# Optimization experiments

Hardware: AMD Instinct MI355X
Metric: run time of the kernel (lower is better)

The kernel has to match this reference:

```python
import jax, jax.numpy as jnp
import numpy as np

EPS = 1e-12
N_WAY, N_SHOT, C_IN, H_IN, W_IN = 5, 5, 640, 24, 24
TOP_LR = 0.8


def _normalize(x, axis):
    # torch F.normalize: x / max(||x||_2, eps)
    n = jnp.sqrt(jnp.sum(x * x, axis=axis, keepdims=True))
    return x / jnp.maximum(n, EPS)


def _conv1x1(x, W, b):
    # x: (B,C,H,W), W: (O,C), b: (O,)
    return jnp.einsum('bchw,oc->bohw', x, W) + b[None, :, None, None]


def _attlayer(x, Wc, bc, Wq, bq, Wk, bk):
    B, C, H, W = x.shape
    HW = H * W
    n_way, n_shot = N_WAY, N_SHOT
    scale = 1.0 / (C ** 0.5)
    x5 = _conv1x1(x, Wc, bc) + x
    x5 = _conv1x1(x5, Wq, bq)            # note: query_transform applied here
    # query_transform applied AGAIN (faithful to original)
    xq = _conv1x1(x5, Wq, bq).reshape(n_way, n_shot, C, HW)
    x_query = jnp.swapaxes(xq, 2, 3).reshape(n_way, n_shot * HW, C)
    xk = _conv1x1(x5, Wk, bk).reshape(n_way, n_shot, C, HW)
    x_key = jnp.swapaxes(xk, 1, 2).reshape(n_way, C, n_shot * HW)
    x_w1 = jnp.matmul(x_query, x_key) * scale          # (n_way, n_shot*HW, n_shot*HW)
    x_w = x_w1.reshape(n_way, n_shot * HW, n_shot, HW).max(-1).mean(-1)
    x_w = jax.nn.softmax(x_w.reshape(n_way, n_shot, HW), axis=-1)
    norm0 = _normalize(x5, 1).reshape(n_way, n_shot, C, H, W)
    # hard-max mask over spatial positions
    mask = (x_w == x_w.max(-1, keepdims=True)).astype(x.dtype)   # (n_way, n_shot, HW)
    seeds = (norm0 * mask.reshape(n_way, n_shot, 1, H, W)).sum((3, 4))  # (n_way, n_shot, C)
    # conv3d with 1x1 spatial kernel over full channel depth == einsum
    cor = jnp.einsum('nkcyx,okc->noyx', norm0, seeds).reshape(n_way, n_shot, HW)
    cmin = cor.min(-1, keepdims=True)
    cmax = cor.max(-1, keepdims=True)
    cor = (cor - cmin) / (cmax - cmin + EPS)
    cormap = cor.reshape(n_way * n_shot, 1, H, W)
    x51 = (x5 * cormap).reshape(n_way, n_shot, C, H, W)
    return x51.mean((1, 3, 4))  # (n_way, C)


def _cdsnet(lf):
    B, C, H, W = lf.shape
    HW = H * W
    n_way, n_shot = N_WAY, N_SHOT
    lfn = _normalize(lf, 1)
    X = jnp.swapaxes(lfn.reshape(B, C, HW), 1, 2)          # (B, HW, C)
    intra = X.reshape(n_way, n_shot * HW, C)
    # d_intra: masked (1-eye) gram mean == (x_i . S_way - ||x_i||^2)/(n_shot*HW)
    S_way = intra.sum(1)                                    # (n_way, C)
    d_intra = (jnp.einsum('nic,nc->ni', intra, S_way) - (intra * intra).sum(-1)) / (n_shot * HW)
    # d_inter: block-diagonal (same-image) pairs masked out
    S_tot = X.sum((0, 1))                                   # (C,)
    S_img = X.sum(1)                                        # (B, C)
    d_inter = (jnp.einsum('bic,c->bi', X, S_tot) - jnp.einsum('bic,bc->bi', X, S_img)) / (B * HW)
    cds = jax.nn.sigmoid(d_intra.reshape(n_way, -1) / d_inter.reshape(n_way, -1))  # (n_way, n_shot*HW)
    k = int(n_shot * HW * TOP_LR)
    _, sel_idx = jax.lax.top_k(cds, k)
    sel = jnp.zeros((n_way, n_shot * HW), lf.dtype)
    sel = sel.at[jnp.arange(n_way)[:, None], sel_idx].set(1.0)
    pos_small = sel.reshape(n_way * n_shot, 1, H, W)
    slf = lf * pos_small                                    # select_local_features
    slf_n = jnp.swapaxes(_normalize(slf.reshape(B, C, HW), 1), 1, 2)
    slf_n = slf_n.reshape(n_way, n_shot, HW, C)
    m1 = slf_n.reshape(n_way, n_shot * HW, C).mean(1)       # (n_way, C)
    l_intra = jnp.matmul(m1, m1.T) * (1.0 - jnp.eye(n_way, dtype=lf.dtype))
    m2 = slf_n.mean(2)                                      # (n_way, n_shot, C)
    l_inter = jnp.einsum('nsc,ntc->nst', m2, m2) * (1.0 - jnp.eye(n_shot, dtype=lf.dtype))
    loss = jnp.exp(l_inter.mean() / l_intra.mean())
    pos_index = jnp.broadcast_to(pos_small, (B, C, H, W))
    neg_index = 1.0 - pos_index
    return loss, pos_index, neg_index


def setup_inputs() -> dict:
    key = jax.random.key(0)
    ks = jax.random.split(key, 7)
    C = C_IN
    s = N_WAY * N_SHOT
    scale = 1.0 / np.sqrt(C)
    lf = jax.random.normal(ks[0], (s, C, H_IN, W_IN), jnp.float32)
    Wc = jax.random.normal(ks[1], (C, C), jnp.float32) * scale
    bc = jax.random.normal(ks[2], (C,), jnp.float32) * 0.01
    Wq = jax.random.normal(ks[3], (C, C), jnp.float32) * scale
    bq = jax.random.normal(ks[4], (C,), jnp.float32) * 0.01
    Wk = jax.random.normal(ks[5], (C, C), jnp.float32) * scale
    bk = jax.random.normal(ks[6], (C,), jnp.float32) * 0.01
    return {'local_feature': lf, 'Wc': Wc, 'bc': bc, 'Wq': Wq, 'bq': bq, 'Wk': Wk, 'bk': bk}


def reference(local_feature, Wc, bc, Wq, bq, Wk, bk):
    s, c, h, w = local_feature.shape
    hw = h * w
    proto1 = _attlayer(local_feature, Wc, bc, Wq, bq, Wk, bk)   # (n_way, C)
    global_proto = jnp.broadcast_to(proto1[:, None, :], (N_WAY, N_SHOT, c)).reshape(s, c)
    gpa = global_proto[:, None, :]                               # (s, 1, C) -> broadcasts to (s, HW, C)
    contrastive_loss, pos_index, neg_index = _cdsnet(local_feature)
    pos_x = _normalize(jnp.swapaxes((local_feature * pos_index).reshape(s, c, hw), 1, 2), -1)
    neg_x = _normalize(jnp.swapaxes((local_feature * neg_index).reshape(s, c, hw), 1, 2), -1)
    pos_value = jnp.exp(pos_x * gpa).sum(-1).mean(-1).mean(-1)
    neg_value = jnp.exp(neg_x * gpa).sum(-1).mean(-1).mean(-1)
    ctc_loss = -jnp.log(pos_value / neg_value)
    return (contrastive_loss, ctc_loss, pos_index)
```

## Files before the change

### kernel.cpp

```cpp
#include <hip/hip_runtime.h>
#include <math.h>

#define NW 5
#define NS 5
#define BB 25
#define CD 640
#define HWD 576
#define NP 2880
#define KTOP 2304
#define EPSF 1e-12f

typedef __attribute__((ext_vector_type(8))) short short8;
typedef __attribute__((ext_vector_type(4))) float f32x4;

__device__ inline unsigned short f2bf(float x) {
    unsigned u = __float_as_uint(x);
    return (unsigned short)((u + 0x7fffu + ((u >> 16) & 1u)) >> 16);
}
__device__ inline float bf2f(unsigned short h) { return __uint_as_float(((unsigned)h) << 16); }

__device__ inline void gload_lds16(const void* g, void* l) {
    __builtin_amdgcn_global_load_lds(
        (const __attribute__((address_space(1))) unsigned int*)g,
        (__attribute__((address_space(3))) unsigned int*)l, 16, 0, 0);
}

__device__ void dev_gemm640(const float* __restrict__ A, const float* __restrict__ B,
                            const float* __restrict__ add, float* __restrict__ C,
                            unsigned short* __restrict__ H, unsigned short* __restrict__ L,
                            int mode, int bx, int by, char* smem)
{
    float (*At)[68] = (float(*)[68])smem;
    float (*Bt)[64] = (float(*)[64])(smem + 8704);
    const int o0 = by * 64, j0 = bx * 64;
    const int t  = threadIdx.x;
    const int to = (t >> 4) * 4, tj = (t & 15) * 4;

    float acc[4][4];
#pragma unroll
    for (int r = 0; r < 4; ++r)
#pragma unroll
        for (int s = 0; s < 4; ++s) acc[r][s] = 0.f;

    for (int c0 = 0; c0 < CD; c0 += 32) {
        __syncthreads();
        {
            const int r = t >> 3, c8 = (t & 7) * 8;
            float4 b0 = *(const float4*)&B[(size_t)(c0+r)*CD + j0 + c8];
            float4 b1 = *(const float4*)&B[(size_t)(c0+r)*CD + j0 + c8 + 4];
            *(float4*)&Bt[r][c8]     = b0;
            *(float4*)&Bt[r][c8 + 4] = b1;
            if (mode == 0) {
                float4 a0 = *(const float4*)&A[(size_t)(c0+r)*CD + o0 + c8];
                float4 a1 = *(const float4*)&A[(size_t)(c0+r)*CD + o0 + c8 + 4];
                *(float4*)&At[r][c8]     = a0;
                *(float4*)&At[r][c8 + 4] = a1;
            } else {
                const int r2 = t >> 2, c82 = (t & 3) * 8;
                float4 a0 = *(const float4*)&A[(size_t)(o0+r2)*CD + c0 + c82];
                float4 a1 = *(const float4*)&A[(size_t)(o0+r2)*CD + c0 + c82 + 4];
                At[c82+0][r2] = a0.x; At[c82+1][r2] = a0.y;
                At[c82+2][r2] = a0.z; At[c82+3][r2] = a0.w;
                At[c82+4][r2] = a1.x; At[c82+5][r2] = a1.y;
                At[c82+6][r2] = a1.z; At[c82+7][r2] = a1.w;
            }
        }
        __syncthreads();
#pragma unroll
        for (int kk = 0; kk < 32; ++kk) {
            float4 av = *(const float4*)&At[kk][to];
            float4 bv = *(const float4*)&Bt[kk][tj];
            float aa[4] = {av.x, av.y, av.z, av.w};
            float bb[4] = {bv.x, bv.y, bv.z, bv.w};
#pragma unroll
            for (int r = 0; r < 4; ++r)
#pragma unroll
                for (int s = 0; s < 4; ++s)
                    acc[r][s] = fmaf(aa[r], bb[s], acc[r][s]);
        }
    }

#pragma unroll
    for (int r = 0; r < 4; ++r) {
        float v[4] = {acc[r][0], acc[r][1], acc[r][2], acc[r][3]};
        const size_t base = (size_t)(o0+to+r)*CD + j0 + tj;
        if (add != nullptr) {
            float4 ad = *(const float4*)&add[base];
            v[0] += ad.x; v[1] += ad.y; v[2] += ad.z; v[3] += ad.w;
        }
        if (C != nullptr) {
            float4 o4; o4.x = v[0]; o4.y = v[1]; o4.z = v[2]; o4.w = v[3];
            *(float4*)&C[base] = o4;
        }
        if (H != nullptr) {
            ushort4 h, l;
            h.x = f2bf(v[0]); h.y = f2bf(v[1]); h.z = f2bf(v[2]); h.w = f2bf(v[3]);
            l.x = f2bf(v[0] - bf2f(h.x)); l.y = f2bf(v[1] - bf2f(h.y));
            l.z = f2bf(v[2] - bf2f(h.z)); l.w = f2bf(v[3] - bf2f(h.w));
            *(ushort4*)&H[base] = h; *(ushort4*)&L[base] = l;
        }
    }
}

__device__ void dev_convert(const float* __restrict__ in, unsigned short* __restrict__ Oh,
                            unsigned short* __restrict__ Ol, int b, int xidx, char* smem)
{
    float (*tile)[65] = (float(*)[65])smem;
    const int c0 = (xidx / 9) * 64;
    const int p0 = (xidx % 9) * 64;
    const int t  = threadIdx.x;
    const float* src = in + (size_t)b * CD * HWD;
#pragma unroll
    for (int it = 0; it < 4; ++it) {
        int cl = (t >> 4) + 16*it, pl = (t & 15) * 4;
        float4 v = *(const float4*)&src[(size_t)(c0+cl)*HWD + p0 + pl];
        tile[cl][pl] = v.x; tile[cl][pl+1] = v.y; tile[cl][pl+2] = v.z; tile[cl][pl+3] = v.w;
    }
    __syncthreads();
#pragma unroll
    for (int it = 0; it < 4; ++it) {
        int pl = (t >> 4) + 16*it, clb = (t & 15) * 4;
        ushort4 hv, lv;
        float x0 = tile[clb+0][pl], x1 = tile[clb+1][pl], x2 = tile[clb+2][pl], x3 = tile[clb+3][pl];
        hv.x = f2bf(x0); hv.y = f2bf(x1); hv.z = f2bf(x2); hv.w = f2bf(x3);
        lv.x = f2bf(x0 - bf2f(hv.x)); lv.y = f2bf(x1 - bf2f(hv.y));
        lv.z = f2bf(x2 - bf2f(hv.z)); lv.w = f2bf(x3 - bf2f(hv.w));
        size_t o = (size_t)(b*HWD + p0 + pl) * CD + c0 + clb;
        *(ushort4*)&Oh[o] = hv;
        *(ushort4*)&Ol[o] = lv;
    }
}

__global__ __launch_bounds__(256) void prep_a(
    const float* __restrict__ lf, const float* __restrict__ Wc,
    const float* __restrict__ bc, const float* __restrict__ Wq,
    const float* __restrict__ bq, const float* __restrict__ Wk,
    const float* __restrict__ bk,
    float* __restrict__ M2, float* __restrict__ Weff,
    float* __restrict__ wqtbk, float* __restrict__ bqwk, float* __restrict__ beff,
    float* __restrict__ sbb,
    unsigned short* __restrict__ lfTh, unsigned short* __restrict__ lfTl,
    float* __restrict__ cor, float* __restrict__ sumsq, float* __restrict__ rvsum,
    float* __restrict__ proto1, float* __restrict__ scal, float* __restrict__ invnl)
{
    __shared__ __align__(16) char smem[16896];
    const int blk = blockIdx.x;
    const int t = threadIdx.x;
    if (blk < 100) {
        dev_gemm640(Wq, Wk, nullptr, M2, nullptr, nullptr, 0, blk % 10, blk / 10, smem);
    } else if (blk < 200) {
        int b2 = blk - 100;
        dev_gemm640(Wq, Wc, Wq, Weff, nullptr, nullptr, 1, b2 % 10, b2 / 10, smem);
    } else if (blk < 210) {
        const int o = (blk - 200)*64 + (t >> 2);
        const int m0 = (t & 3) * 160;
        float s1 = 0.f, s2 = 0.f;
        for (int m = m0; m < m0 + 160; ++m) {
            s1 = fmaf(Wq[(size_t)m*CD + o], bk[m], s1);
            s2 = fmaf(bq[m], Wk[(size_t)m*CD + o], s2);
        }
        s1 += __shfl_xor(s1, 1, 64); s1 += __shfl_xor(s1, 2, 64);
        s2 += __shfl_xor(s2, 1, 64); s2 += __shfl_xor(s2, 2, 64);
        if ((t & 3) == 0) { wqtbk[o] = s1; bqwk[o] = s2; }
    } else if (blk < 220) {
        const int o = (blk - 210)*64 + (t >> 2);
        const int m0 = (t & 3) * 160;
        const float* ap = Wq + (size_t)o*CD + m0;
        float a = 0.f;
        for (int m = 0; m < 160; ++m) a = fmaf(ap[m], bc[m0 + m], a);
        a += __shfl_xor(a, 1, 64); a += __shfl_xor(a, 2, 64);
        if ((t & 3) == 0) beff[o] = a + bq[o];
    } else if (blk == 220) {
        __shared__ float red[4];
        float a = 0.f;
        for (int m = t; m < CD; m += 256) a = fmaf(bq[m], bk[m], a);
        for (int off2 = 32; off2; off2 >>= 1) a += __shfl_down(a, off2, 64);
        if ((t & 63) == 0) red[t >> 6] = a;
        __syncthreads();
        if (t == 0) sbb[0] = red[0] + red[1] + red[2] + red[3];
    } else if (blk < 2471) {
        const int idx = blk - 221;
        dev_convert(lf, lfTh, lfTl, idx / 90, idx % 90, smem);
    } else if (blk < 2503) {
        const int i0 = (blk - 2471)*256 + t;
        for (int i = i0; i < 14400; i += 8192) { cor[i] = 0.f; sumsq[i] = 0.f; rvsum[i] = 0.f; }
        for (int i = i0; i < 3200; i += 8192) proto1[i] = 0.f;
        if (i0 < 2) scal[i0] = 0.f;
    } else {
        const int idx = blk - 2503;
        const int pb = idx % 9, b = idx / 9;
        const int p = pb*64 + (t >> 2);
        const int cb = (t & 3) * 160;
        const float* sp = lf + (size_t)b*CD*HWD + p + (size_t)cb*HWD;
        float a = 0.f;
        for (int c = 0; c < 160; ++c) { float v = sp[(size_t)c*HWD]; a = fmaf(v, v, a); }
        a += __shfl_xor(a, 1, 64); a += __shfl_xor(a, 2, 64);
        if ((t & 3) == 0) invnl[b*HWD + p] = 1.f / fmaxf(sqrtf(a), EPSF);
    }
}

__global__ __launch_bounds__(256) void prep_b(
    const float* __restrict__ M2, const float* __restrict__ Weff,
    const float* __restrict__ beff, const float* __restrict__ wqtbk,
    unsigned short* __restrict__ WeH, unsigned short* __restrict__ WeL,
    unsigned short* __restrict__ MeH, unsigned short* __restrict__ MeL,
    float* __restrict__ wbias)
{
    __shared__ __align__(16) char smem[16896];
    const int blk = blockIdx.x;
    const int t = threadIdx.x;
    if (blk < 100) {
        dev_gemm640(M2, Weff, nullptr, nullptr, MeH, MeL, 1, blk % 10, blk / 10, smem);
    } else if (blk < 200) {
        int i = (blk - 100)*256 + t;
        float4 v = ((const float4*)Weff)[i];
        ushort4 h, l;
        h.x = f2bf(v.x); h.y = f2bf(v.y); h.z = f2bf(v.z); h.w = f2bf(v.w);
        l.x = f2bf(v.x - bf2f(h.x)); l.y = f2bf(v.y - bf2f(h.y));
        l.z = f2bf(v.z - bf2f(h.z)); l.w = f2bf(v.w - bf2f(h.w));
        ((ushort4*)WeH)[i] = h; ((ushort4*)WeL)[i] = l;
    } else {
        const int o = (blk - 200)*64 + (t >> 2);
        const int m0 = (t & 3) * 160;
        const float* ap = M2 + (size_t)o*CD + m0;
        float a = 0.f;
        for (int m = 0; m < 160; ++m) a = fmaf(ap[m], beff[m0 + m], a);
        a += __shfl_xor(a, 1, 64); a += __shfl_xor(a, 2, 64);
        if ((t & 3) == 0) wbias[o] = a + wqtbk[o];
    }
}

__global__ __launch_bounds__(256) void conv2x(
    const unsigned short* __restrict__ Ah_, const unsigned short* __restrict__ Al_,
    const unsigned short* __restrict__ WeH, const unsigned short* __restrict__ WeL,
    const unsigned short* __restrict__ MeH, const unsigned short* __restrict__ MeL,
    const float* __restrict__ beff, const float* __restrict__ wbias,
    const float* __restrict__ bqwk,
    unsigned short* __restrict__ x5h, unsigned short* __restrict__ x5l,
    unsigned short* __restrict__ wh,  unsigned short* __restrict__ wl,
    float* __restrict__ sumsq, float* __restrict__ rvsum)
{
    __shared__ __align__(16) unsigned short lds[14336];
    const int obx  = blockIdx.x;
    const int osel = (obx < 5);
    const int o0   = (osel ? obx : obx - 5) * 128;
    const unsigned short* Wh = osel ? WeH : MeH;
    const unsigned short* Wl = osel ? WeL : MeL;
    const float* bias = osel ? beff : wbias;
    unsigned short* Oh = osel ? x5h : wh;
    unsigned short* Ol = osel ? x5l : wl;
    const int row0 = blockIdx.y * 96;
    const int t    = threadIdx.x;
    const int w    = t >> 6, lane = t & 63;
    const int ihalf = (w & 1) * 48;
    const int jhalf = (w >> 1) * 64;

    f32x4 acc[3][4];
#pragma unroll
    for (int f = 0; f < 3; ++f)
#pragma unroll
        for (int g = 0; g < 4; ++g) acc[f][g] = (f32x4){0.f,0.f,0.f,0.f};

    const int rl = lane >> 2;
    const int cl = (lane & 3) * 8;

    for (int c0 = 0; c0 < CD; c0 += 32) {
#pragma unroll
        for (int e = 0; e < 7; ++e) {
            const int s = w*7 + e;
            const unsigned short* src;
            if (s < 6)        src = Ah_ + (size_t)(row0 + s*16      + rl)*CD + c0 + cl;
            else if (s < 12)  src = Al_ + (size_t)(row0 + (s-6)*16  + rl)*CD + c0 + cl;
            else if (s < 20)  src = Wh  + (size_t)(o0   + (s-12)*16 + rl)*CD + c0 + cl;
            else              src = Wl  + (size_t)(o0   + (s-20)*16 + rl)*CD + c0 + cl;
            gload_lds16(src, &lds[s*512]);
        }
        __syncthreads();

        const int chunk = (lane >> 4) * 8;
        short8 afh[3], afl[3];
#pragma unroll
        for (int f = 0; f < 3; ++f) {
            int row = ihalf + f*16 + (lane & 15);
            afh[f] = *(const short8*)&lds[row*32 + chunk];
            afl[f] = *(const short8*)&lds[3072 + row*32 + chunk];
        }
#pragma unroll
        for (int g = 0; g < 4; ++g) {
            int row = jhalf + g*16 + (lane & 15);
            short8 bfh = *(const short8*)&lds[6144  + row*32 + chunk];
            short8 bfl = *(const short8*)&lds[10240 + row*32 + chunk];
#pragma unroll
            for (int f = 0; f < 3; ++f) {
                acc[f][g] = __builtin_amdgcn_mfma_f32_16x16x32_bf16(afh[f], bfh, acc[f][g], 0, 0, 0);
                acc[f][g] = __builtin_amdgcn_mfma_f32_16x16x32_bf16(afh[f], bfl, acc[f][g], 0, 0, 0);
                acc[f][g] = __builtin_amdgcn_mfma_f32_16x16x32_bf16(afl[f], bfh, acc[f][g], 0, 0, 0);
            }
        }
        __syncthreads();
    }

    float bs[4], bw[4];
#pragma unroll
    for (int g = 0; g < 4; ++g) {
        const int o = o0 + jhalf + g*16 + (lane & 15);
        bs[g] = bias[o];
        bw[g] = osel ? bqwk[o] : 0.f;
    }
#pragma unroll
    for (int f = 0; f < 3; ++f) {
        const int rbase = row0 + ihalf + f*16 + (lane >> 4)*4;
#pragma unroll
        for (int r = 0; r < 4; ++r) {
            float sq = 0.f, rv = 0.f;
#pragma unroll
            for (int g = 0; g < 4; ++g) {
                const int o = o0 + jhalf + g*16 + (lane & 15);
                const size_t idx = (size_t)(rbase + r)*CD + o;
                float v = acc[f][g][r] + bs[g];
                unsigned short hi = f2bf(v);
                Oh[idx] = hi;
                Ol[idx] = f2bf(v - bf2f(hi));
                sq = fmaf(v, v, sq);
                rv = fmaf(v, bw[g], rv);
            }
            if (osel) {
                sq += __shfl_xor(sq, 1, 64); rv += __shfl_xor(rv, 1, 64);
                sq += __shfl_xor(sq, 2, 64); rv += __shfl_xor(rv, 2, 64);
                sq += __shfl_xor(sq, 4, 64); rv += __shfl_xor(rv, 4, 64);
                sq += __shfl_xor(sq, 8, 64); rv += __shfl_xor(rv, 8, 64);
                if ((lane & 15) == 0) {
                    atomicAdd(&sumsq[rbase + r], sq);
                    atomicAdd(&rvsum[rbase + r], rv);
                }
            }
        }
    }
}

__global__ __launch_bounds__(256) void qk_mega(
    const unsigned short* __restrict__ Qh, const unsigned short* __restrict__ Ql,
    const unsigned short* __restrict__ Kh, const unsigned short* __restrict__ Kl,
    const float* __restrict__ rvsum, const float* __restrict__ sbb,
    const float* __restrict__ lf, const float* __restrict__ invnl,
    float* __restrict__ xwp, float* __restrict__ S_img)
{
    __shared__ __align__(16) unsigned short lds[18432];
    const int blk = blockIdx.x;
    const int t   = threadIdx.x;
    if (blk >= 2250) {
        const int i = blk - 2250;
        const int ct = i % 160, b = i / 160;
        const int pi = t & 63, cj = t >> 6;
        const int c = ct * 4 + cj;
        const float* xp = lf + ((size_t)b * CD + c) * HWD;
        const float* ip = invnl + b * HWD;
        float acc = 0.f;
        for (int p = pi; p < HWD; p += 64) acc = fmaf(xp[p], ip[p], acc);
        for (int off = 32; off; off >>= 1) acc += __shfl_down(acc, off, 64);
        if (pi == 0) S_img[b * CD + c] = acc;
        return;
    }
    const int n    = blk / 450;
    const int yy   = (blk / 30) % 15;
    const int i0   = (blk % 30) * 96;
    const int shot = yy / 3;
    const int jt   = yy % 3;
    const int w    = t >> 6, lane = t & 63;
    const int ihalf = (w & 1) * 48;
    const int jhalf = (w >> 1) * 96;

    const size_t qbase = (size_t)(n*NP + i0) * CD;
    const size_t kbase = (size_t)(n*NP + shot*HWD + jt*192) * CD;

    f32x4 acc[3][6];
#pragma unroll
    for (int f = 0; f < 3; ++f)
#pragma unroll
        for (int g = 0; g < 6; ++g) acc[f][g] = (f32x4){0.f,0.f,0.f,0.f};

    const int rl = lane >> 2;
    const int cl = (lane & 3) * 8;

    for (int c0 = 0; c0 < CD; c0 += 32) {
#pragma unroll
        for (int e = 0; e < 9; ++e) {
            const int s = w*9 + e;
            const int r = s*16 + rl;
            const unsigned short* src;
            if (s < 6)        src = Qh + qbase + (size_t)r*CD        + c0 + cl;
            else if (s < 12)  src = Ql + qbase + (size_t)(r-96)*CD   + c0 + cl;
            else if (s < 24)  src = Kh + kbase + (size_t)(r-192)*CD  + c0 + cl;
            else              src = Kl + kbase + (size_t)(r-384)*CD  + c0 + cl;
            gload_lds16(src, &lds[s*512]);
        }
        __syncthreads();

        const int chunk = (lane >> 4) * 8;
        short8 afh[3], afl[3];
#pragma unroll
        for (int f = 0; f < 3; ++f) {
            int row = ihalf + f*16 + (lane & 15);
            afh[f] = *(const short8*)&lds[row*32 + chunk];
            afl[f] = *(const short8*)&lds[3072 + row*32 + chunk];
        }
#pragma unroll
        for (int g = 0; g < 6; ++g) {
            int row = jhalf + g*16 + (lane & 15);
            short8 bfh = *(const short8*)&lds[6144  + row*32 + chunk];
            short8 bfl = *(const short8*)&lds[12288 + row*32 + chunk];
#pragma unroll
            for (int f = 0; f < 3; ++f) {
                acc[f][g] = __builtin_amdgcn_mfma_f32_16x16x32_bf16(afh[f], bfh, acc[f][g], 0, 0, 0);
                acc[f][g] = __builtin_amdgcn_mfma_f32_16x16x32_bf16(afh[f], bfl, acc[f][g], 0, 0, 0);
                acc[f][g] = __builtin_amdgcn_mfma_f32_16x16x32_bf16(afl[f], bfh, acc[f][g], 0, 0, 0);
            }
        }
        __syncthreads();
    }

    const float sv = sbb[0];
    float rv[6];
    {
        int jg0 = n*NP + shot*HWD + jt*192 + jhalf + (lane & 15);
#pragma unroll
        for (int g = 0; g < 6; ++g) rv[g] = rvsum[jg0 + g*16] + sv;
    }
    float* smax = (float*)lds;
#pragma unroll
    for (int f = 0; f < 3; ++f) {
#pragma unroll
        for (int r = 0; r < 4; ++r) {
            float m = -INFINITY;
#pragma unroll
            for (int g = 0; g < 6; ++g) m = fmaxf(m, acc[f][g][r] + rv[g]);
#pragma unroll
            for (int off = 1; off < 16; off <<= 1) m = fmaxf(m, __shfl_xor(m, off, 64));
            if ((lane & 15) == 0) smax[(ihalf + f*16 + (lane >> 4)*4 + r)*2 + (w >> 1)] = m;
        }
    }
    __syncthreads();
    if (t < 96) {
        float m = fmaxf(smax[t*2], smax[t*2 + 1]);
        xwp[(((size_t)n*5 + shot)*3 + jt)*NP + i0 + t] = m;
    }
}

__global__ __launch_bounds__(256) void post_1(
    const float* __restrict__ xwp,
    const unsigned short* __restrict__ Xh, const unsigned short* __restrict__ Xl,
    const float* __restrict__ sumsq, const float* __restrict__ S_img,
    float* __restrict__ seeds, float* __restrict__ S_way, float* __restrict__ S_tot)
{
    const int blk = blockIdx.x;
    const int t = threadIdx.x;
    if (blk < 25) {
        const int b = blk;
        const int n = b / NS, sq = b % NS;
        __shared__ float wv[4]; __shared__ int wi[4]; __shared__ int spix;
        float bv = -INFINITY; int bi = 0x7fffffff;
        for (int p = t; p < HWD; p += 256) {
            const int i = sq * HWD + p;
            float v = 0.f;
#pragma unroll
            for (int s = 0; s < NS; ++s) {
                float m = -INFINITY;
#pragma unroll
                for (int tt = 0; tt < 3; ++tt)
                    m = fmaxf(m, xwp[(((size_t)(n*NS+s))*3 + tt)*NP + i]);
                v += m;
            }
            if (v > bv) { bv = v; bi = p; }
        }
        const int lane = t & 63, w = t >> 6;
        for (int off = 32; off; off >>= 1) {
            float ov = __shfl_down(bv, off, 64);
            int   oi = __shfl_down(bi, off, 64);
            if (ov > bv || (ov == bv && oi < bi)) { bv = ov; bi = oi; }
        }
        if (lane == 0) { wv[w] = bv; wi[w] = bi; }
        __syncthreads();
        if (t == 0) {
            float best = wv[0]; int bidx = wi[0];
            for (int k = 1; k < 4; ++k)
                if (wv[k] > best || (wv[k] == best && wi[k] < bidx)) { best = wv[k]; bidx = wi[k]; }
            spix = bidx;
        }
        __syncthreads();
        const int row = b*HWD + spix;
        const float in1 = 1.f / fmaxf(sqrtf(sumsq[row]), EPSF);
        for (int c = t; c < CD; c += 256) {
            float v = bf2f(Xh[(size_t)row*CD + c]) + bf2f(Xl[(size_t)row*CD + c]);
            seeds[b*CD + c] = v * in1;
        }
        return;
    }
    for (int c = t; c < CD; c += 256) {
        float tot = 0.f;
        for (int nn = 0; nn < NW; ++nn) {
            float w2 = 0.f;
            for (int s = 0; s < NS; ++s) w2 += S_img[(nn*NS+s)*CD + c];
            S_way[nn*CD + c] = w2; tot += w2;
        }
        S_tot[c] = tot;
    }
}

__global__ __launch_bounds__(256) void post_2(
    const unsigned short* __restrict__ Xh, const unsigned short* __restrict__ Xl,
    const float* __restrict__ sumsq, const float* __restrict__ seeds,
    const float* __restrict__ lf, const float* __restrict__ invnl,
    const float* __restrict__ S_way, const float* __restrict__ S_img,
    const float* __restrict__ S_tot,
    float* __restrict__ cor, float* __restrict__ cds)
{
    const int blk = blockIdx.x;
    const int t = threadIdx.x;
    if (blk < 900) {
        const int zc = blk / 225, rem = blk % 225;
        const int pb = rem % 9, b = rem / 9;
        const int n = b / NS, k = b % NS;
        const int p = pb*64 + (t >> 2);
        const int row = b*HWD + p;
        const int cb = zc*160 + (t & 3) * 40;
        const unsigned short* ph = Xh + (size_t)row*CD + cb;
        const unsigned short* pl = Xl + (size_t)row*CD + cb;
        float a[5] = {0.f,0.f,0.f,0.f,0.f};
        for (int c = 0; c < 40; c += 8) {
            short8 h8 = *(const short8*)&ph[c];
            short8 l8 = *(const short8*)&pl[c];
#pragma unroll
            for (int j = 0; j < 8; ++j) {
                float v = bf2f((unsigned short)h8[j]) + bf2f((unsigned short)l8[j]);
#pragma unroll
                for (int o = 0; o < 5; ++o)
                    a[o] = fmaf(v, seeds[(o*NS + k)*CD + cb + c + j], a[o]);
            }
        }
        const float in1 = 1.f / fmaxf(sqrtf(sumsq[row]), EPSF);
#pragma unroll
        for (int o = 0; o < 5; ++o) {
            float s = a[o];
            s += __shfl_xor(s, 1, 64); s += __shfl_xor(s, 2, 64);
            if ((t & 3) == 0) atomicAdd(&cor[(n*5 + o)*HWD + p], in1 * s);
        }
        return;
    }
    const int idx = blk - 900;
    const int pb = idx % 9, b = idx / 9;
    const int p = pb*64 + (t >> 2);
    const int cb = (t & 3) * 160;
    const int n = b / NS;
    const float* xp = lf + (size_t)b*CD*HWD + p + (size_t)cb*HWD;
    const float* wv = S_way + n*CD + cb;
    const float* iv = S_img + b*CD + cb;
    const float* tv = S_tot + cb;
    float dw = 0.f, di = 0.f, dt = 0.f, sq = 0.f;
    for (int c = 0; c < 160; ++c) {
        float v = xp[(size_t)c*HWD];
        dw = fmaf(v, wv[c], dw);
        di = fmaf(v, iv[c], di);
        dt = fmaf(v, tv[c], dt);
        sq = fmaf(v, v, sq);
    }
    dw += __shfl_xor(dw,1,64); dw += __shfl_xor(dw,2,64);
    di += __shfl_xor(di,1,64); di += __shfl_xor(di,2,64);
    dt += __shfl_xor(dt,1,64); dt += __shfl_xor(dt,2,64);
    sq += __shfl_xor(sq,1,64); sq += __shfl_xor(sq,2,64);
    if ((t & 3) == 0) {
        float in1 = invnl[b*HWD + p];
        float d_intra = (in1 * dw - in1 * in1 * sq) * (1.f / 2880.f);
        float d_inter = (in1 * dt - in1 * di) * (1.f / 14400.f);
        float r = d_intra / d_inter;
        cds[n * NP + (b % NS) * HWD + p] = 1.f / (1.f + expf(-r));
    }
}

__global__ __launch_bounds__(576) void post_3(
    const float* __restrict__ cds,
    const unsigned short* __restrict__ Xh, const unsigned short* __restrict__ Xl,
    const float* __restrict__ cor,
    float* __restrict__ sel, float* __restrict__ proto1)
{
    __shared__ unsigned int u[NP];
    __shared__ int hist[256];
    __shared__ int red[16];
    __shared__ int bcast;
    __shared__ unsigned sprefix;
    __shared__ int skk;
    __shared__ int scanbuf[576];
    __shared__ float corb[NP];
    __shared__ float sacc[576];
    __shared__ float mnv[5], mxv[5];
    const int blk = blockIdx.x;
    const int t = threadIdx.x;
    if (blk >= 5) {
        const int idx = blk - 5;
        const int n = idx / 10, ct = idx % 10;
        for (int j = t; j < NP; j += 576) corb[j] = cor[n*NP + j];
        __syncthreads();
        if (t < 320) {
            const int o = t >> 6, lane = t & 63;
            float mn = INFINITY, mx = -INFINITY;
            for (int j = lane; j < HWD; j += 64) {
                float v = corb[o*HWD + j];
                mn = fminf(mn, v); mx = fmaxf(mx, v);
            }
            for (int off = 32; off; off >>= 1) {
                mn = fminf(mn, __shfl_xor(mn, off, 64));
                mx = fmaxf(mx, __shfl_xor(mx, off, 64));
            }
            if (lane == 0) { mnv[o] = mn; mxv[o] = mx; }
        }
        __syncthreads();
        for (int j = t; j < NP; j += 576) {
            int o = j / HWD;
            corb[j] = (corb[j] - mnv[o]) / (mxv[o] - mnv[o] + EPSF);
        }
        __syncthreads();
        const int c = ct*64 + (t & 63);
        const int rc = t >> 6;
        float a = 0.f;
        for (int rr = rc*320; rr < rc*320 + 320; ++rr) {
            size_t row = (size_t)(n*NP + rr);
            float v = bf2f(Xh[row*CD + c]) + bf2f(Xl[row*CD + c]);
            a = fmaf(v, corb[rr], a);
        }
        sacc[t] = a;
        __syncthreads();
        if (t < 64) {
            float s = 0.f;
            for (int q = 0; q < 9; ++q) s += sacc[t + 64*q];
            proto1[n*CD + ct*64 + t] = s * (1.f / 2880.f);
        }
        return;
    }
    const int n = blk;
    for (int j = t; j < NP; j += 576) {
        unsigned int x = __float_as_uint(cds[n * NP + j]);
        u[j] = (x & 0x80000000u) ? ~x : (x | 0x80000000u);
    }
    if (t == 0) { skk = KTOP; sprefix = 0u; }
    __syncthreads();
    const int j0 = t * 5;
    for (int byte = 3; byte >= 0; --byte) {
        if (t < 256) hist[t] = 0;
        __syncthreads();
        const int sh = byte * 8;
        const unsigned pmask = (byte == 3) ? 0u : (0xFFFFFFFFu << (sh + 8));
        const unsigned pref = sprefix;
#pragma unroll
        for (int e = 0; e < 5; ++e) {
            unsigned v = u[j0+e];
            if ((v & pmask) == pref) atomicAdd(&hist[(v >> sh) & 255], 1);
        }
        __syncthreads();
        if (t == 0) {
            int kk = skk, acc = 0, b2;
            for (b2 = 255; b2 >= 0; --b2) { acc += hist[b2]; if (acc >= kk) break; }
            skk = kk - (acc - hist[b2]);
            sprefix = pref | ((unsigned)b2 << sh);
        }
        __syncthreads();
    }
    const unsigned int T = sprefix;
    int cg = 0, ce = 0;
#pragma unroll
    for (int e = 0; e < 5; ++e) {
        unsigned v = u[j0+e];
        if (v > T) cg++; else if (v == T) ce++;
    }
    const int lane = t & 63, w = t >> 6;
    int r1 = cg;
    for (int off = 32; off; off >>= 1) r1 += __shfl_down(r1, off, 64);
    if (lane == 0) red[w] = r1;
    __syncthreads();
    if (t == 0) { int s2 = 0; for (int q = 0; q < 9; ++q) s2 += red[q]; bcast = s2; }
    __syncthreads();
    const int need = KTOP - bcast;
    scanbuf[t] = ce;
    __syncthreads();
    for (int off = 1; off < 576; off <<= 1) {
        int v2 = (t >= off) ? scanbuf[t - off] : 0;
        __syncthreads();
        scanbuf[t] += v2;
        __syncthreads();
    }
    int excl = scanbuf[t] - ce;
    int eidx = 0;
#pragma unroll
    for (int e = 0; e < 5; ++e) {
        int j = j0 + e;
        unsigned v = u[j];
        float s = 0.f;
        if (v > T) s = 1.f;
        else if (v == T) { if (excl + eidx < need) s = 1.f; eidx++; }
        int sh2 = j / HWD;
        sel[(n*NS + sh2) * HWD + (j - sh2*HWD)] = s;
    }
}

__global__ __launch_bounds__(256) void post_4(
    const float* __restrict__ lf, const float* __restrict__ invnl,
    const float* __restrict__ sel, const float* __restrict__ proto1,
    float* __restrict__ Sm, float* __restrict__ scal, float* __restrict__ out)
{
    const int blk = blockIdx.x;
    const int t = threadIdx.x;
    if (blk < 4000) {
        const int ct = blk % 160, b = blk / 160;
        const int pi = t & 63, cj = t >> 6;
        const int c = ct * 4 + cj;
        const float* xp = lf + ((size_t)b * CD + c) * HWD;
        const float* ip = invnl + b * HWD;
        const float* mp = sel + b * HWD;
        float acc = 0.f;
        for (int p = pi; p < HWD; p += 64) acc = fmaf(xp[p], ip[p] * mp[p], acc);
        for (int off = 32; off; off >>= 1) acc += __shfl_down(acc, off, 64);
        if (pi == 0) Sm[b * CD + c] = acc;
        return;
    }
    if (blk < 4225) {
        const int i = blk - 4000;
        const int pb = i % 9, b = i / 9;
        const int p = pb*64 + (t >> 2);
        const int cb = (t & 3) * 160;
        const int n = b / NS;
        const float* xp = lf + (size_t)b*CD*HWD + p + (size_t)cb*HWD;
        const float* pr = proto1 + n*CD + cb;
        float in1 = invnl[b*HWD + p];
        float acc = 0.f;
        for (int c = 0; c < 160; ++c) acc += expf(xp[(size_t)c*HWD] * in1 * pr[c]);
        acc += __shfl_xor(acc, 1, 64); acc += __shfl_xor(acc, 2, 64);
        float pv = 0.f, nv = 0.f;
        if ((t & 3) == 0) {
            float s = sel[b*HWD + p];
            pv = (s > 0.5f) ? acc : 640.f;
            nv = (s > 0.5f) ? 640.f : acc;
        }
        for (int off = 32; off >= 4; off >>= 1) {
            pv += __shfl_down(pv, off, 64);
            nv += __shfl_down(nv, off, 64);
        }
        if ((t & 63) == 0) { atomicAdd(&scal[0], pv); atomicAdd(&scal[1], nv); }
        return;
    }
    int idx = (blk - 4225) * 256 + t;
    int row = idx / 144;
    int f4  = idx - row * 144;
    int b   = row / CD;
    const float* sp = sel + b * HWD + f4 * 4;
    float* op = out + 2 + (size_t)row * HWD + f4 * 4;
    float2 v0 = make_float2(sp[0], sp[1]);
    float2 v1 = make_float2(sp[2], sp[3]);
    *(float2*)op = v0; *(float2*)(op + 2) = v1;
}

__global__ __launch_bounds__(256) void fin_kernel(
    const float* __restrict__ Sm, const float* __restrict__ scal,
    float* __restrict__ out)
{
    const int blk = blockIdx.x;
    const int t = threadIdx.x;
    if (blk == 1) {
        if (t == 0) out[1] = -(logf(scal[0]) - logf(scal[1]));
        return;
    }
    __shared__ double sa[4], sb2[4], sc[4];
    double A = 0.0, Bv = 0.0, Cv = 0.0;
    for (int c = t; c < CD; c += 256) {
        float tot = 0.f;
        for (int nn = 0; nn < NW; ++nn) {
            float ws = 0.f;
            for (int s = 0; s < NS; ++s) {
                float v = Sm[(nn*NS+s)*CD + c];
                ws += v; Cv += (double)v * v;
            }
            tot += ws; A += (double)ws * ws;
        }
        Bv += (double)tot * tot;
    }
    const int lane = t & 63, w = t >> 6;
    for (int off = 32; off; off >>= 1) {
        A  += __shfl_down(A,  off, 64);
        Bv += __shfl_down(Bv, off, 64);
        Cv += __shfl_down(Cv, off, 64);
    }
    if (lane == 0) { sa[w] = A; sb2[w] = Bv; sc[w] = Cv; }
    __syncthreads();
    if (t == 0) {
        double a = 0, b2 = 0, cc = 0;
        for (int q = 0; q < 4; ++q) { a += sa[q]; b2 += sb2[q]; cc += sc[q]; }
        out[0] = (float)exp(5.0 * (a - cc) / (b2 - a));
    }
}

extern "C" void kernel_launch(void* const* d_in, const int* in_sizes, int n_in,
                              void* d_out, int out_size, void* d_ws, size_t ws_size,
                              hipStream_t stream) {
    const float* lf = (const float*)d_in[0];
    const float* Wc = (const float*)d_in[1];
    const float* bc = (const float*)d_in[2];
    const float* Wq = (const float*)d_in[3];
    const float* bq = (const float*)d_in[4];
    const float* Wk = (const float*)d_in[5];
    const float* bk = (const float*)d_in[6];
    float* out = (float*)d_out;
    float* ws = (float*)d_ws;

    const size_t FEAT = 9216000;
    size_t off = 0;
    auto alloc = [&](size_t nf) { float* p = ws + off; off += (nf + 3) & ~(size_t)3; return p; };
    float* s0     = alloc(FEAT);
    float* s1     = alloc(FEAT);
    float* xwp    = alloc(216000);
    float* seeds  = alloc(16000);
    float* invnl  = alloc(14400);
    float* sumsq  = alloc(14400);
    float* rvsum  = alloc(14400);
    float* cor    = alloc(14400);
    float* proto1 = alloc(3200);
    float* S_img  = alloc(16000);
    float* S_way  = alloc(3200);
    float* S_tot  = alloc(640);
    float* cds    = alloc(14400);
    float* sel    = alloc(14400);
    float* Sm     = alloc(16000);
    float* scal   = alloc(8);
    float* wqtbk  = alloc(640);
    float* bqwk   = alloc(640);
    float* sbb    = alloc(4);
    float* beff   = alloc(640);
    float* wbias  = alloc(640);
    float* WeS    = alloc(409600);
    float* MeS    = alloc(409600);

    float* M2   = s1;
    float* Weff = s1 + 409600;

    unsigned short* WeH = (unsigned short*)WeS; unsigned short* WeL = WeH + 409600;
    unsigned short* MeH = (unsigned short*)MeS; unsigned short* MeL = MeH + 409600;

    unsigned short* lfTh = (unsigned short*)(out + 2);
    unsigned short* lfTl = lfTh + FEAT;

    unsigned short* s0h = (unsigned short*)s0; unsigned short* s0l = s0h + FEAT;
    unsigned short* s1h = (unsigned short*)s1; unsigned short* s1l = s1h + FEAT;

    prep_a<<<2728, 256, 0, stream>>>(lf, Wc, bc, Wq, bq, Wk, bk,
                                     M2, Weff, wqtbk, bqwk, beff, sbb,
                                     lfTh, lfTl, cor, sumsq, rvsum, proto1, scal, invnl);
    prep_b<<<210, 256, 0, stream>>>(M2, Weff, beff, wqtbk, WeH, WeL, MeH, MeL, wbias);
    conv2x<<<dim3(10,150), 256, 0, stream>>>(lfTh, lfTl, WeH, WeL, MeH, MeL,
                                             beff, wbias, bqwk,
                                             s0h, s0l, s1h, s1l, sumsq, rvsum);
    qk_mega<<<6250, 256, 0, stream>>>(s0h, s0l, s1h, s1l, rvsum, sbb,
                                      lf, invnl, xwp, S_img);
    post_1<<<26, 256, 0, stream>>>(xwp, s0h, s0l, sumsq, S_img, seeds, S_way, S_tot);
    post_2<<<1125, 256, 0, stream>>>(s0h, s0l, sumsq, seeds, lf, invnl,
                                     S_way, S_img, S_tot, cor, cds);
    post_3<<<55, 576, 0, stream>>>(cds, s0h, s0l, cor, sel, proto1);
    post_4<<<13225, 256, 0, stream>>>(lf, invnl, sel, proto1, Sm, scal, out);
    fin_kernel<<<2, 256, 0, stream>>>(Sm, scal, out);
}
```

Before: 639.5 us.

## Rebalance side work across kernels and replace zero-init blocks with memset

Moves independent side computations into earlier kernels so they run alongside the main GEMMs. S_img goes into conv2x, S_way/S_tot into qk_mega, the cds pass into post_1, and cor accumulation with top-k selection into post_2. proto1 and Sm now run together in post_3, and the exp-sum pass is split four ways over channels. Buffer zeroing is replaced by a hipMemsetAsync on a contiguous region. The aim is to fill idle compute units during small tail phases and raise parallelism in the short post kernels, at the cost of more atomics and one extra memset launch.

```diff
diff --git a/kernel.cpp b/kernel.cpp
--- a/kernel.cpp
+++ b/kernel.cpp
@@ -140,8 +140,7 @@
     float* __restrict__ wqtbk, float* __restrict__ bqwk, float* __restrict__ beff,
     float* __restrict__ sbb,
     unsigned short* __restrict__ lfTh, unsigned short* __restrict__ lfTl,
-    float* __restrict__ cor, float* __restrict__ sumsq, float* __restrict__ rvsum,
-    float* __restrict__ proto1, float* __restrict__ scal, float* __restrict__ invnl)
+    float* __restrict__ invnl)
 {
     __shared__ __align__(16) char smem[16896];
     const int blk = blockIdx.x;
@@ -181,13 +180,8 @@
     } else if (blk < 2471) {
         const int idx = blk - 221;
         dev_convert(lf, lfTh, lfTl, idx / 90, idx % 90, smem);
-    } else if (blk < 2503) {
-        const int i0 = (blk - 2471)*256 + t;
-        for (int i = i0; i < 14400; i += 8192) { cor[i] = 0.f; sumsq[i] = 0.f; rvsum[i] = 0.f; }
-        for (int i = i0; i < 3200; i += 8192) proto1[i] = 0.f;
-        if (i0 < 2) scal[i0] = 0.f;
     } else {
-        const int idx = blk - 2503;
+        const int idx = blk - 2471;
         const int pb = idx % 9, b = idx / 9;
         const int p = pb*64 + (t >> 2);
         const int cb = (t & 3) * 160;
@@ -236,12 +230,28 @@
     const unsigned short* __restrict__ MeH, const unsigned short* __restrict__ MeL,
     const float* __restrict__ beff, const float* __restrict__ wbias,
     const float* __restrict__ bqwk,
+    const float* __restrict__ lf, const float* __restrict__ invnl,
     unsigned short* __restrict__ x5h, unsigned short* __restrict__ x5l,
     unsigned short* __restrict__ wh,  unsigned short* __restrict__ wl,
-    float* __restrict__ sumsq, float* __restrict__ rvsum)
+    float* __restrict__ sumsq, float* __restrict__ rvsum, float* __restrict__ S_img)
 {
     __shared__ __align__(16) unsigned short lds[14336];
-    const int obx  = blockIdx.x;
+    const int blk = blockIdx.x;
+    const int t   = threadIdx.x;
+    if (blk >= 1500) {
+        const int i = blk - 1500;
+        const int ct = i % 160, b = i / 160;
+        const int pi = t & 63, cj = t >> 6;
+        const int c = ct * 4 + cj;
+        const float* xp = lf + ((size_t)b * CD + c) * HWD;
+        const float* ip = invnl + b * HWD;
+        float acc2 = 0.f;
+        for (int p = pi; p < HWD; p += 64) acc2 = fmaf(xp[p], ip[p], acc2);
+        for (int off = 32; off; off >>= 1) acc2 += __shfl_down(acc2, off, 64);
+        if (pi == 0) S_img[b * CD + c] = acc2;
+        return;
+    }
+    const int obx  = blk % 10;
     const int osel = (obx < 5);
     const int o0   = (osel ? obx : obx - 5) * 128;
     const unsigned short* Wh = osel ? WeH : MeH;
@@ -249,8 +259,7 @@
     const float* bias = osel ? beff : wbias;
     unsigned short* Oh = osel ? x5h : wh;
     unsigned short* Ol = osel ? x5l : wl;
-    const int row0 = blockIdx.y * 96;
-    const int t    = threadIdx.x;
+    const int row0 = (blk / 10) * 96;
     const int w    = t >> 6, lane = t & 63;
     const int ihalf = (w & 1) * 48;
     const int jhalf = (w >> 1) * 64;
@@ -342,23 +351,22 @@
     const unsigned short* __restrict__ Qh, const unsigned short* __restrict__ Ql,
     const unsigned short* __restrict__ Kh, const unsigned short* __restrict__ Kl,
     const float* __restrict__ rvsum, const float* __restrict__ sbb,
-    const float* __restrict__ lf, const float* __restrict__ invnl,
-    float* __restrict__ xwp, float* __restrict__ S_img)
+    const float* __restrict__ S_img,
+    float* __restrict__ xwp, float* __restrict__ S_way, float* __restrict__ S_tot)
 {
     __shared__ __align__(16) unsigned short lds[18432];
     const int blk = blockIdx.x;
     const int t   = threadIdx.x;
-    if (blk >= 2250) {
-        const int i = blk - 2250;
-        const int ct = i % 160, b = i / 160;
-        const int pi = t & 63, cj = t >> 6;
-        const int c = ct * 4 + cj;
-        const float* xp = lf + ((size_t)b * CD + c) * HWD;
-        const float* ip = invnl + b * HWD;
-        float acc = 0.f;
-        for (int p = pi; p < HWD; p += 64) acc = fmaf(xp[p], ip[p], acc);
-        for (int off = 32; off; off >>= 1) acc += __shfl_down(acc, off, 64);
-        if (pi == 0) S_img[b * CD + c] = acc;
+    if (blk == 2250) {
+        for (int c = t; c < CD; c += 256) {
+            float tot = 0.f;
+            for (int nn = 0; nn < NW; ++nn) {
+                float w2 = 0.f;
+                for (int s = 0; s < NS; ++s) w2 += S_img[(nn*NS+s)*CD + c];
+                S_way[nn*CD + c] = w2; tot += w2;
+            }
+            S_tot[c] = tot;
+        }
         return;
     }
     const int n    = blk / 450;
@@ -449,8 +457,11 @@
 __global__ __launch_bounds__(256) void post_1(
     const float* __restrict__ xwp,
     const unsigned short* __restrict__ Xh, const unsigned short* __restrict__ Xl,
-    const float* __restrict__ sumsq, const float* __restrict__ S_img,
-    float* __restrict__ seeds, float* __restrict__ S_way, float* __restrict__ S_tot)
+    const float* __restrict__ sumsq,
+    const float* __restrict__ lf, const float* __restrict__ invnl,
+    const float* __restrict__ S_way, const float* __restrict__ S_img,
+    const float* __restrict__ S_tot,
+    float* __restrict__ seeds, float* __restrict__ cds)
 {
     const int blk = blockIdx.x;
     const int t = threadIdx.x;
@@ -495,58 +506,7 @@
         }
         return;
     }
-    for (int c = t; c < CD; c += 256) {
-        float tot = 0.f;
-        for (int nn = 0; nn < NW; ++nn) {
-            float w2 = 0.f;
-            for (int s = 0; s < NS; ++s) w2 += S_img[(nn*NS+s)*CD + c];
-            S_way[nn*CD + c] = w2; tot += w2;
-        }
-        S_tot[c] = tot;
-    }
-}
-
-__global__ __launch_bounds__(256) void post_2(
-    const unsigned short* __restrict__ Xh, const unsigned short* __restrict__ Xl,
-    const float* __restrict__ sumsq, const float* __restrict__ seeds,
-    const float* __restrict__ lf, const float* __restrict__ invnl,
-    const float* __restrict__ S_way, const float* __restrict__ S_img,
-    const float* __restrict__ S_tot,
-    float* __restrict__ cor, float* __restrict__ cds)
-{
-    const int blk = blockIdx.x;
-    const int t = threadIdx.x;
-    if (blk < 900) {
-        const int zc = blk / 225, rem = blk % 225;
-        const int pb = rem % 9, b = rem / 9;
-        const int n = b / NS, k = b % NS;
-        const int p = pb*64 + (t >> 2);
-        const int row = b*HWD + p;
-        const int cb = zc*160 + (t & 3) * 40;
-        const unsigned short* ph = Xh + (size_t)row*CD + cb;
-        const unsigned short* pl = Xl + (size_t)row*CD + cb;
-        float a[5] = {0.f,0.f,0.f,0.f,0.f};
-        for (int c = 0; c < 40; c += 8) {
-            short8 h8 = *(const short8*)&ph[c];
-            short8 l8 = *(const short8*)&pl[c];
-#pragma unroll
-            for (int j = 0; j < 8; ++j) {
-                float v = bf2f((unsigned short)h8[j]) + bf2f((unsigned short)l8[j]);
-#pragma unroll
-                for (int o = 0; o < 5; ++o)
-                    a[o] = fmaf(v, seeds[(o*NS + k)*CD + cb + c + j], a[o]);
-            }
-        }
-        const float in1 = 1.f / fmaxf(sqrtf(sumsq[row]), EPSF);
-#pragma unroll
-        for (int o = 0; o < 5; ++o) {
-            float s = a[o];
-            s += __shfl_xor(s, 1, 64); s += __shfl_xor(s, 2, 64);
-            if ((t & 3) == 0) atomicAdd(&cor[(n*5 + o)*HWD + p], in1 * s);
-        }
-        return;
-    }
-    const int idx = blk - 900;
+    const int idx = blk - 25;
     const int pb = idx % 9, b = idx / 9;
     const int p = pb*64 + (t >> 2);
     const int cb = (t & 3) * 160;
@@ -576,11 +536,11 @@
     }
 }
 
-__global__ __launch_bounds__(576) void post_3(
+__global__ __launch_bounds__(576) void post_2(
+    const unsigned short* __restrict__ Xh, const unsigned short* __restrict__ Xl,
+    const float* __restrict__ sumsq, const float* __restrict__ seeds,
     const float* __restrict__ cds,
-    const unsigned short* __restrict__ Xh, const unsigned short* __restrict__ Xl,
-    const float* __restrict__ cor,
-    float* __restrict__ sel, float* __restrict__ proto1)
+    float* __restrict__ cor, float* __restrict__ sel)
 {
     __shared__ unsigned int u[NP];
     __shared__ int hist[256];
@@ -589,53 +549,39 @@
     __shared__ unsigned sprefix;
     __shared__ int skk;
     __shared__ int scanbuf[576];
-    __shared__ float corb[NP];
-    __shared__ float sacc[576];
-    __shared__ float mnv[5], mxv[5];
     const int blk = blockIdx.x;
     const int t = threadIdx.x;
-    if (blk >= 5) {
-        const int idx = blk - 5;
-        const int n = idx / 10, ct = idx % 10;
-        for (int j = t; j < NP; j += 576) corb[j] = cor[n*NP + j];
-        __syncthreads();
-        if (t < 320) {
-            const int o = t >> 6, lane = t & 63;
-            float mn = INFINITY, mx = -INFINITY;
-            for (int j = lane; j < HWD; j += 64) {
-                float v = corb[o*HWD + j];
-                mn = fminf(mn, v); mx = fmaxf(mx, v);
-            }
-            for (int off = 32; off; off >>= 1) {
-                mn = fminf(mn, __shfl_xor(mn, off, 64));
-                mx = fmaxf(mx, __shfl_xor(mx, off, 64));
-            }
-            if (lane == 0) { mnv[o] = mn; mxv[o] = mx; }
-        }
-        __syncthreads();
-        for (int j = t; j < NP; j += 576) {
-            int o = j / HWD;
-            corb[j] = (corb[j] - mnv[o]) / (mxv[o] - mnv[o] + EPSF);
-        }
-        __syncthreads();
-        const int c = ct*64 + (t & 63);
-        const int rc = t >> 6;
-        float a = 0.f;
-        for (int rr = rc*320; rr < rc*320 + 320; ++rr) {
-            size_t row = (size_t)(n*NP + rr);
-            float v = bf2f(Xh[row*CD + c]) + bf2f(Xl[row*CD + c]);
-            a = fmaf(v, corb[rr], a);
-        }
-        sacc[t] = a;
-        __syncthreads();
-        if (t < 64) {
-            float s = 0.f;
-            for (int q = 0; q < 9; ++q) s += sacc[t + 64*q];
-            proto1[n*CD + ct*64 + t] = s * (1.f / 2880.f);
+    if (blk < 400) {
+        const int zc = blk / 100, rem = blk % 100;
+        const int pb = rem % 4, b = rem / 4;
+        const int n = b / NS, k = b % NS;
+        const int p = pb*144 + (t >> 2);
+        const int row = b*HWD + p;
+        const int cb = zc*160 + (t & 3) * 40;
+        const unsigned short* ph = Xh + (size_t)row*CD + cb;
+        const unsigned short* pl = Xl + (size_t)row*CD + cb;
+        float a[5] = {0.f,0.f,0.f,0.f,0.f};
+        for (int c = 0; c < 40; c += 8) {
+            short8 h8 = *(const short8*)&ph[c];
+            short8 l8 = *(const short8*)&pl[c];
+#pragma unroll
+            for (int j = 0; j < 8; ++j) {
+                float v = bf2f((unsigned short)h8[j]) + bf2f((unsigned short)l8[j]);
+#pragma unroll
+                for (int o = 0; o < 5; ++o)
+                    a[o] = fmaf(v, seeds[(o*NS + k)*CD + cb + c + j], a[o]);
+            }
+        }
+        const float in1 = 1.f / fmaxf(sqrtf(sumsq[row]), EPSF);
+#pragma unroll
+        for (int o = 0; o < 5; ++o) {
+            float s = a[o];
+            s += __shfl_xor(s, 1, 64); s += __shfl_xor(s, 2, 64);
+            if ((t & 3) == 0) atomicAdd(&cor[(n*5 + o)*HWD + p], in1 * s);
         }
         return;
     }
-    const int n = blk;
+    const int n = blk - 400;
     for (int j = t; j < NP; j += 576) {
         unsigned int x = __float_as_uint(cds[n * NP + j]);
         u[j] = (x & 0x80000000u) ? ~x : (x | 0x80000000u);
@@ -700,43 +646,96 @@
     }
 }
 
+__global__ __launch_bounds__(256) void post_3(
+    const unsigned short* __restrict__ Xh, const unsigned short* __restrict__ Xl,
+    const float* __restrict__ cor,
+    const float* __restrict__ lf, const float* __restrict__ invnl,
+    const float* __restrict__ sel,
+    float* __restrict__ proto1, float* __restrict__ Sm)
+{
+    const int blk = blockIdx.x;
+    const int t = threadIdx.x;
+    if (blk < 50) {
+        __shared__ float corb[NP];
+        __shared__ float sacc[256];
+        __shared__ float mnv[5], mxv[5];
+        const int n = blk / 10, ct = blk % 10;
+        for (int j = t; j < NP; j += 256) corb[j] = cor[n*NP + j];
+        __syncthreads();
+        {
+            const int lane = t & 63;
+            for (int o = t >> 6; o < 5; o += 4) {
+                float mn = INFINITY, mx = -INFINITY;
+                for (int j = lane; j < HWD; j += 64) {
+                    float v = corb[o*HWD + j];
+                    mn = fminf(mn, v); mx = fmaxf(mx, v);
+                }
+                for (int off = 32; off; off >>= 1) {
+                    mn = fminf(mn, __shfl_xor(mn, off, 64));
+                    mx = fmaxf(mx, __shfl_xor(mx, off, 64));
+                }
+                if (lane == 0) { mnv[o] = mn; mxv[o] = mx; }
+            }
+        }
+        __syncthreads();
+        for (int j = t; j < NP; j += 256) {
+            int o = j / HWD;
+            corb[j] = (corb[j] - mnv[o]) / (mxv[o] - mnv[o] + EPSF);
+        }
+        __syncthreads();
+        const int c = ct*64 + (t & 63);
+        const int rc = t >> 6;
+        float a = 0.f;
+        for (int rr = rc*720; rr < rc*720 + 720; ++rr) {
+            size_t row = (size_t)(n*NP + rr);
+            float v = bf2f(Xh[row*CD + c]) + bf2f(Xl[row*CD + c]);
+            a = fmaf(v, corb[rr], a);
+        }
+        sacc[t] = a;
+        __syncthreads();
+        if (t < 64) {
+            float s = sacc[t] + sacc[t+64] + sacc[t+128] + sacc[t+192];
+            proto1[n*CD + c] = s * (1.f / 2880.f);
+        }
+        return;
+    }
+    const int i = blk - 50;
+    const int ct = i % 160, b = i / 160;
+    const int pi = t & 63, cj = t >> 6;
+    const int c = ct * 4 + cj;
+    const float* xp = lf + ((size_t)b * CD + c) * HWD;
+    const float* ip = invnl + b * HWD;
+    const float* mp = sel + b * HWD;
+    float acc = 0.f;
+    for (int p = pi; p < HWD; p += 64) acc = fmaf(xp[p], ip[p] * mp[p], acc);
+    for (int off = 32; off; off >>= 1) acc += __shfl_down(acc, off, 64);
+    if (pi == 0) Sm[b * CD + c] = acc;
+}
+
 __global__ __launch_bounds__(256) void post_4(
     const float* __restrict__ lf, const float* __restrict__ invnl,
     const float* __restrict__ sel, const float* __restrict__ proto1,
-    float* __restrict__ Sm, float* __restrict__ scal, float* __restrict__ out)
+    float* __restrict__ scal, float* __restrict__ out)
 {
     const int blk = blockIdx.x;
     const int t = threadIdx.x;
-    if (blk < 4000) {
-        const int ct = blk % 160, b = blk / 160;
-        const int pi = t & 63, cj = t >> 6;
-        const int c = ct * 4 + cj;
-        const float* xp = lf + ((size_t)b * CD + c) * HWD;
-        const float* ip = invnl + b * HWD;
-        const float* mp = sel + b * HWD;
-        float acc = 0.f;
-        for (int p = pi; p < HWD; p += 64) acc = fmaf(xp[p], ip[p] * mp[p], acc);
-        for (int off = 32; off; off >>= 1) acc += __shfl_down(acc, off, 64);
-        if (pi == 0) Sm[b * CD + c] = acc;
-        return;
-    }
-    if (blk < 4225) {
-        const int i = blk - 4000;
-        const int pb = i % 9, b = i / 9;
+    if (blk < 900) {
+        const int zc = blk / 225, rem = blk % 225;
+        const int pb = rem % 9, b = rem / 9;
         const int p = pb*64 + (t >> 2);
-        const int cb = (t & 3) * 160;
+        const int cb = zc*160 + (t & 3) * 40;
         const int n = b / NS;
         const float* xp = lf + (size_t)b*CD*HWD + p + (size_t)cb*HWD;
         const float* pr = proto1 + n*CD + cb;
         float in1 = invnl[b*HWD + p];
         float acc = 0.f;
-        for (int c = 0; c < 160; ++c) acc += expf(xp[(size_t)c*HWD] * in1 * pr[c]);
+        for (int c = 0; c < 40; ++c) acc += expf(xp[(size_t)c*HWD] * in1 * pr[c]);
         acc += __shfl_xor(acc, 1, 64); acc += __shfl_xor(acc, 2, 64);
         float pv = 0.f, nv = 0.f;
         if ((t & 3) == 0) {
             float s = sel[b*HWD + p];
-            pv = (s > 0.5f) ? acc : 640.f;
-            nv = (s > 0.5f) ? 640.f : acc;
+            pv = (s > 0.5f) ? acc : 160.f;
+            nv = (s > 0.5f) ? 160.f : acc;
         }
         for (int off = 32; off >= 4; off >>= 1) {
             pv += __shfl_down(pv, off, 64);
@@ -745,7 +744,7 @@
         if ((t & 63) == 0) { atomicAdd(&scal[0], pv); atomicAdd(&scal[1], nv); }
         return;
     }
-    int idx = (blk - 4225) * 256 + t;
+    int idx = (blk - 900) * 256 + t;
     int row = idx / 144;
     int f4  = idx - row * 144;
     int b   = row / CD;
@@ -816,9 +815,12 @@
     float* xwp    = alloc(216000);
     float* seeds  = alloc(16000);
     float* invnl  = alloc(14400);
+    float* zbase  = alloc(0);
+    float* cor    = alloc(14400);
     float* sumsq  = alloc(14400);
     float* rvsum  = alloc(14400);
-    float* cor    = alloc(14400);
+    float* scal   = alloc(8);
+    const size_t zbytes = (14400*3 + 8) * sizeof(float);
     float* proto1 = alloc(3200);
     float* S_img  = alloc(16000);
     float* S_way  = alloc(3200);
@@ -826,7 +828,6 @@
     float* cds    = alloc(14400);
     float* sel    = alloc(14400);
     float* Sm     = alloc(16000);
-    float* scal   = alloc(8);
     float* wqtbk  = alloc(640);
     float* bqwk   = alloc(640);
     float* sbb    = alloc(4);
@@ -847,19 +848,20 @@
     unsigned short* s0h = (unsigned short*)s0; unsigned short* s0l = s0h + FEAT;
     unsigned short* s1h = (unsigned short*)s1; unsigned short* s1l = s1h + FEAT;
 
-    prep_a<<<2728, 256, 0, stream>>>(lf, Wc, bc, Wq, bq, Wk, bk,
+    hipMemsetAsync(zbase, 0, zbytes, stream);
+    prep_a<<<2696, 256, 0, stream>>>(lf, Wc, bc, Wq, bq, Wk, bk,
                                      M2, Weff, wqtbk, bqwk, beff, sbb,
-                                     lfTh, lfTl, cor, sumsq, rvsum, proto1, scal, invnl);
+                                     lfTh, lfTl, invnl);
     prep_b<<<210, 256, 0, stream>>>(M2, Weff, beff, wqtbk, WeH, WeL, MeH, MeL, wbias);
-    conv2x<<<dim3(10,150), 256, 0, stream>>>(lfTh, lfTl, WeH, WeL, MeH, MeL,
-                                             beff, wbias, bqwk,
-                                             s0h, s0l, s1h, s1l, sumsq, rvsum);
-    qk_mega<<<6250, 256, 0, stream>>>(s0h, s0l, s1h, s1l, rvsum, sbb,
-                                      lf, invnl, xwp, S_img);
-    post_1<<<26, 256, 0, stream>>>(xwp, s0h, s0l, sumsq, S_img, seeds, S_way, S_tot);
-    post_2<<<1125, 256, 0, stream>>>(s0h, s0l, sumsq, seeds, lf, invnl,
-                                     S_way, S_img, S_tot, cor, cds);
-    post_3<<<55, 576, 0, stream>>>(cds, s0h, s0l, cor, sel, proto1);
-    post_4<<<13225, 256, 0, stream>>>(lf, invnl, sel, proto1, Sm, scal, out);
+    conv2x<<<5500, 256, 0, stream>>>(lfTh, lfTl, WeH, WeL, MeH, MeL,
+                                     beff, wbias, bqwk, lf, invnl,
+                                     s0h, s0l, s1h, s1l, sumsq, rvsum, S_img);
+    qk_mega<<<2251, 256, 0, stream>>>(s0h, s0l, s1h, s1l, rvsum, sbb, S_img,
+                                      xwp, S_way, S_tot);
+    post_1<<<250, 256, 0, stream>>>(xwp, s0h, s0l, sumsq, lf, invnl,
+                                    S_way, S_img, S_tot, seeds, cds);
+    post_2<<<405, 576, 0, stream>>>(s0h, s0l, sumsq, seeds, cds, cor, sel);
+    post_3<<<4050, 256, 0, stream>>>(s0h, s0l, cor, lf, invnl, sel, proto1, Sm);
+    post_4<<<9900, 256, 0, stream>>>(lf, invnl, sel, proto1, scal, out);
     fin_kernel<<<2, 256, 0, stream>>>(Sm, scal, out);
 }
```

New measurement: 727.6 us. +13.8%, slower.
